# Performance work log

Hardware: AMD Instinct MI355X
Metric: run time of the kernel (lower is better)

Reference implementation:

```python
import jax, jax.numpy as jnp
import numpy as np

N, R, C = 128, 2304, 256  # batch of Stiefel params, each viewed as tall [r, c] (j==6 dispatch: 2304x256)


def setup_inputs() -> dict:
    key = jax.random.key(0)
    k1, k2, k3, k4, k5 = jax.random.split(key, 5)
    M0 = jax.random.normal(k1, (N, R, C), dtype=jnp.float32)
    # project onto the Stiefel manifold (orthonormal columns), as the real optimizer maintains
    M, _ = jnp.linalg.qr(M0)
    M_grad = jax.random.normal(k2, (N, R, C), dtype=jnp.float32)
    update = jax.random.normal(k3, (N, R, C), dtype=jnp.float32)  # stands in for LSTM optimizee output
    lr = jax.random.uniform(k4, (N, 1, 1), dtype=jnp.float32)      # stands in for LSTM-predicted lr
    s_lr = jax.random.uniform(k5, (1,), dtype=jnp.float32)
    return {"M": M, "M_grad": M_grad, "update": update, "lr": lr, "s_lr": s_lr}


def reference(M, M_grad, update, lr, s_lr):
    s = s_lr[0]

    def step(Mi, Gi_raw, Ui, lri):
        # othogonal_projection: G = Gi_raw - M @ sym(M^T @ Gi_raw)
        A = Mi.T @ Gi_raw                      # [c, c]
        A_sym = 0.5 * (A + A.T)
        G = Gi_raw - Mi @ A_sym                # [r, c]
        # update_R = -|lr| * s_lr * (update + G)
        P = -jnp.abs(lri) * s * (Ui + G)
        # retraction: QR with sign fix, then transpose (as in step())
        Q, Rm = jnp.linalg.qr(Mi + P)          # Q: [r, c], Rm: [c, c]
        sgn = jnp.sign(jnp.sign(jnp.diagonal(Rm)) + 0.5)  # (R.diag().sign()+0.5).sign()
        return (Q * sgn[None, :]).T            # [c, r] = retraction(M, P).T

    return jax.vmap(step)(M, M_grad, update, lr[:, 0, 0])
```

## Files before the change

kernel.cpp:

```cpp
#include <hip/hip_runtime.h>
#include <hip/hip_bf16.h>
#include <stdint.h>


typedef _Float16 f16;
typedef _Float16 half4 __attribute__((ext_vector_type(4)));
typedef _Float16 half8 __attribute__((ext_vector_type(8)));
typedef float float4v __attribute__((ext_vector_type(4)));

#define AS1 __attribute__((address_space(1)))
#define AS3 __attribute__((address_space(3)))

__device__ __forceinline__ void gload_lds16(const f16* g, f16* l) {
  __builtin_amdgcn_global_load_lds((const AS1 void*)g, (AS3 void*)l, 16, 0, 0);
}

__global__ __launch_bounds__(256) void prep_kernel(
    const float* __restrict__ M, const float* __restrict__ G,
    const float* __restrict__ U, const float* __restrict__ lr,
    const float* __restrict__ sl,
    f16* __restrict__ M16, f16* __restrict__ Mt,
    f16* __restrict__ Gt,  f16* __restrict__ GU)
{
  __shared__ f16 T[256 * 72];
  const int b = blockIdx.z, mode = blockIdx.y, r0 = blockIdx.x * 64;
  const int tid = threadIdx.x;
  const size_t bin = (size_t)b * 589824;
  const float* src = (mode ? G : M) + bin + (size_t)r0 * 256;
  const float* usrc = U + bin + (size_t)r0 * 256;
  const float cb = mode ? fabsf(lr[b]) * sl[0] : 0.f;

  for (int q = 0; q < 16; ++q) {
    int idx = q * 256 + tid;
    int rr = idx >> 6, c4 = (idx & 63) * 4;
    float4 v = *(const float4*)(src + (size_t)rr * 256 + c4);
    f16 h0 = (f16)v.x, h1 = (f16)v.y, h2 = (f16)v.z, h3 = (f16)v.w;
    T[(c4 + 0) * 72 + rr] = h0;
    T[(c4 + 1) * 72 + rr] = h1;
    T[(c4 + 2) * 72 + rr] = h2;
    T[(c4 + 3) * 72 + rr] = h3;
    if (mode == 0) {
      half4 hv; hv[0] = h0; hv[1] = h1; hv[2] = h2; hv[3] = h3;
      *(half4*)(M16 + bin + (size_t)(r0 + rr) * 256 + c4) = hv;
    } else {
      float4 u = *(const float4*)(usrc + (size_t)rr * 256 + c4);
      half4 gu;
      gu[0] = (f16)(cb * (v.x + u.x));
      gu[1] = (f16)(cb * (v.y + u.y));
      gu[2] = (f16)(cb * (v.z + u.z));
      gu[3] = (f16)(cb * (v.w + u.w));
      *(half4*)(GU + bin + (size_t)(r0 + rr) * 256 + c4) = gu;
    }
  }
  __syncthreads();
  f16* dst = (mode ? Gt : Mt) + bin;
  for (int q = 0; q < 8; ++q) {
    int idx = q * 256 + tid;
    int cc = idx >> 3, r8 = (idx & 7) * 8;
    half8 hv = *(const half8*)(T + cc * 72 + r8);
    *(half8*)(dst + (size_t)cc * 2304 + r0 + r8) = hv;
  }
}

__global__ __launch_bounds__(256) void tranb_kernel(const f16* __restrict__ B,
                                                    f16* __restrict__ Bt)
{
  __shared__ f16 T[256 * 72];
  const int b = blockIdx.z, r0 = blockIdx.x * 64, tid = threadIdx.x;
  const size_t bin = (size_t)b * 589824;
  for (int q = 0; q < 8; ++q) {
    int idx = q * 256 + tid;
    int rr = idx >> 5, c8 = (idx & 31) * 8;
    half8 v = *(const half8*)(B + bin + (size_t)(r0 + rr) * 256 + c8);
#pragma unroll
    for (int i = 0; i < 8; ++i) T[(c8 + i) * 72 + rr] = v[i];
  }
  __syncthreads();
  for (int q = 0; q < 8; ++q) {
    int idx = q * 256 + tid;
    int cc = idx >> 3, r8 = (idx & 7) * 8;
    *(half8*)(Bt + bin + (size_t)cc * 2304 + r0 + r8) =
        *(const half8*)(T + cc * 72 + r8);
  }
}

__global__ __launch_bounds__(256) void symw_kernel(
    const float* __restrict__ A, const float* __restrict__ lr,
    const float* __restrict__ sl, f16* __restrict__ W)
{
  __shared__ float T1[64 * 65];
  __shared__ float T2[64 * 65];
  const int b = blockIdx.z, tid = threadIdx.x;
  int pr = blockIdx.x;
  int ti = 0;
  while ((ti + 1) * (ti + 2) / 2 <= pr) ++ti;
  int tj = pr - ti * (ti + 1) / 2;
  const int i0 = ti * 64, j0 = tj * 64;
  const float* Ab = A + (size_t)b * 65536;
  const float ch = 0.5f * fabsf(lr[b]) * sl[0];

  for (int q = 0; q < 4; ++q) {
    int idx = q * 256 + tid;
    int r = idx >> 4, c4 = (idx & 15) * 4;
    float4 v = *(const float4*)(Ab + (size_t)(i0 + r) * 256 + j0 + c4);
    T1[r * 65 + c4 + 0] = v.x; T1[r * 65 + c4 + 1] = v.y;
    T1[r * 65 + c4 + 2] = v.z; T1[r * 65 + c4 + 3] = v.w;
    if (ti != tj) {
      float4 w = *(const float4*)(Ab + (size_t)(j0 + r) * 256 + i0 + c4);
      T2[r * 65 + c4 + 0] = w.x; T2[r * 65 + c4 + 1] = w.y;
      T2[r * 65 + c4 + 2] = w.z; T2[r * 65 + c4 + 3] = w.w;
    }
  }
  __syncthreads();
  const float* T2p = (ti == tj) ? T1 : T2;
  f16* Wb = W + (size_t)b * 65536;
  for (int q = 0; q < 16; ++q) {
    int idx = q * 256 + tid;
    int r = idx >> 6, c = idx & 63;
    float val = ch * (T1[r * 65 + c] + T2p[c * 65 + r]);
    if (ti == tj && r == c) val += 1.f;
    Wb[(size_t)(i0 + r) * 256 + j0 + c] = (f16)val;
  }
  if (ti != tj) {
    for (int q = 0; q < 16; ++q) {
      int idx = q * 256 + tid;
      int r = idx >> 6, c = idx & 63;
      float val = ch * (T2[r * 65 + c] + T1[c * 65 + r]);
      Wb[(size_t)(j0 + r) * 256 + i0 + c] = (f16)val;
    }
  }
}

template <int EPI>
__global__ __launch_bounds__(256) void gemm_kernel(
    const f16* __restrict__ Abase, long sA, int lda,
    const f16* __restrict__ Bbase, long sB, int ldb, int K,
    float* __restrict__ Cf, long sC, int ldc,
    f16* __restrict__ C16, const f16* __restrict__ GU, long sGU)
{
  __shared__ f16 As[128 * 64];
  __shared__ f16 Bs[128 * 64];
  const int b = blockIdx.z;
  const int tid = threadIdx.x, lane = tid & 63, wave = tid >> 6;
  const int wm = wave >> 1, wn = wave & 1;
  const int quad = lane >> 4, l15 = lane & 15;
  const f16* Ap = Abase + (size_t)b * sA + (size_t)(blockIdx.x * 128) * lda;
  const f16* Bp = Bbase + (size_t)b * sB + (size_t)(blockIdx.y * 128) * ldb;

  float4v acc[4][4];
#pragma unroll
  for (int i = 0; i < 4; ++i)
#pragma unroll
    for (int j = 0; j < 4; ++j)
#pragma unroll
      for (int r = 0; r < 4; ++r) acc[i][j][r] = 0.f;

  for (int kt = 0; kt < K; kt += 64) {
    __syncthreads();
#pragma unroll
    for (int q = 0; q < 4; ++q) {
      int pos = q * 256 + wave * 64 + lane;
      int m = pos >> 3, jc = pos & 7;
      int g = jc ^ (m & 7);
      gload_lds16(Ap + (size_t)m * lda + kt + g * 8,
                  As + (q * 256 + wave * 64) * 8);
      gload_lds16(Bp + (size_t)m * ldb + kt + g * 8,
                  Bs + (q * 256 + wave * 64) * 8);
    }
    __syncthreads();
#pragma unroll
    for (int ks = 0; ks < 2; ++ks) {
      half8 af[4], bf[4];
      int kc = ks * 4 + quad;
#pragma unroll
      for (int i = 0; i < 4; ++i) {
        int m = wm * 64 + i * 16 + l15;
        af[i] = *(const half8*)(As + m * 64 + ((kc ^ (m & 7)) * 8));
        int n = wn * 64 + i * 16 + l15;
        bf[i] = *(const half8*)(Bs + n * 64 + ((kc ^ (n & 7)) * 8));
      }
#pragma unroll
      for (int i = 0; i < 4; ++i)
#pragma unroll
        for (int j = 0; j < 4; ++j)
          acc[i][j] = __builtin_amdgcn_mfma_f32_16x16x32_f16(af[i], bf[j],
                                                             acc[i][j], 0, 0, 0);
    }
  }

#pragma unroll
  for (int i = 0; i < 4; ++i) {
#pragma unroll
    for (int j = 0; j < 4; ++j) {
      int m0 = blockIdx.x * 128 + wm * 64 + i * 16 + quad * 4;
      int n = blockIdx.y * 128 + wn * 64 + j * 16 + l15;
#pragma unroll
      for (int r = 0; r < 4; ++r) {
        int m = m0 + r;
        if constexpr (EPI == 0) {
          Cf[(size_t)b * sC + (size_t)m * ldc + n] = acc[i][j][r];
        } else {
          float v = acc[i][j][r] - (float)GU[(size_t)b * sGU + (size_t)m * 256 + n];
          C16[(size_t)b * sC + (size_t)m * ldc + n] = (f16)v;
        }
      }
    }
  }
}

__global__ __launch_bounds__(1024) void chol_kernel(float* __restrict__ Sg,
                                                    f16* __restrict__ Linv)
{
  __shared__ float Pan[256 * 32];
  __shared__ float Dinv[8 * 528];
  __shared__ float Tscr[32 * 32];
  __shared__ float stash[32];
  const int b = blockIdx.x, tid = threadIdx.x;
  float* Lg = Sg + (size_t)b * 65536;
  f16* Lo = Linv + (size_t)b * 65536;

  for (int t = tid; t < 16384; t += 1024) ((uint64_t*)Lo)[t] = 0ull;

  for (int p = 0; p < 8; ++p) {
    const int c0 = p * 32, rows = 256 - c0;
    __syncthreads();
    for (int t = tid; t < rows * 32; t += 1024) {
      int r = t >> 5, k = t & 31;
      Pan[t] = Lg[(size_t)(c0 + r) * 256 + c0 + k];
    }
    __syncthreads();
    for (int jj = 0; jj < 32; ++jj) {
      int i = jj + tid;
      bool act = (i < rows);
      int i2 = act ? i : jj;
      float pv = Pan[jj * 32 + jj];
      float v = Pan[i2 * 32 + jj];
      for (int k = 0; k < jj; ++k) {
        float ljk = Pan[jj * 32 + k];
        pv -= ljk * ljk;
        v -= Pan[i2 * 32 + k] * ljk;
      }
      float d = sqrtf(fmaxf(pv, 1e-20f));
      float rd = 1.f / d;
      if (act) {
        if (tid == 0) stash[jj] = d;
        else Pan[i * 32 + jj] = v * rd;
      }
      __syncthreads();
    }
    if (tid < 32) Pan[tid * 32 + tid] = stash[tid];
    __syncthreads();
    for (int t = tid; t < rows * 32; t += 1024) {
      int r = t >> 5, k = t & 31;
      Lg[(size_t)(c0 + r) * 256 + c0 + k] = Pan[t];
    }
    int R = 256 - (c0 + 32);
    if (R > 0) {
      int nb = R >> 3, nblk = nb * (nb + 1) / 2;
      for (int bx = tid; bx < nblk; bx += 1024) {
        int br = (int)((sqrtf(8.f * bx + 1.f) - 1.f) * 0.5f);
        while ((br + 1) * (br + 2) / 2 <= bx) ++br;
        while (br * (br + 1) / 2 > bx) --br;
        int bc = bx - br * (br + 1) / 2;
        int il = 32 + br * 8, jl = 32 + bc * 8;
        float acc[8][8];
#pragma unroll
        for (int r = 0; r < 8; ++r) {
          const float* cp = Lg + (size_t)(c0 + il + r) * 256 + c0 + jl;
#pragma unroll
          for (int c = 0; c < 8; ++c) acc[r][c] = cp[c];
        }
        for (int k = 0; k < 32; ++k) {
          float a[8], bb[8];
#pragma unroll
          for (int r = 0; r < 8; ++r) a[r] = Pan[(il + r) * 32 + k];
#pragma unroll
          for (int c = 0; c < 8; ++c) bb[c] = Pan[(jl + c) * 32 + k];
#pragma unroll
          for (int r = 0; r < 8; ++r)
#pragma unroll
            for (int c = 0; c < 8; ++c) acc[r][c] -= a[r] * bb[c];
        }
#pragma unroll
        for (int r = 0; r < 8; ++r) {
          float* cp = Lg + (size_t)(c0 + il + r) * 256 + c0 + jl;
#pragma unroll
          for (int c = 0; c < 8; ++c) cp[c] = acc[r][c];
        }
      }
    }
  }
  __syncthreads();

  if (tid < 256) {
    int w = tid >> 5, c = tid & 31;
    const float* Lb = Lg + (size_t)(32 * w) * 256 + 32 * w;
    for (int i = c; i < 32; ++i) {
      float s = (i == c) ? 1.f : 0.f;
      for (int k = c; k < i; ++k)
        s -= Lb[i * 256 + k] * Dinv[w * 528 + k * (k + 1) / 2 + c];
      Dinv[w * 528 + i * (i + 1) / 2 + c] = s / Lb[i * 256 + i];
    }
  }
  __syncthreads();

  for (int p = 0; p < 8; ++p) {
    {
      int i = tid >> 5, k = tid & 31;
      float val = (k <= i) ? Dinv[p * 528 + i * (i + 1) / 2 + k] : 0.f;
      Pan[i * 32 + k] = val;
      Lo[(size_t)(32 * p + i) * 256 + 32 * p + k] = (f16)val;
    }
    __syncthreads();
    for (int r = p + 1; r < 8; ++r) {
      int i = tid >> 5, j = tid & 31;
      float s = 0.f;
      for (int a = p; a < r; ++a) {
        const float* Lrow = Lg + (size_t)(32 * r + i) * 256 + 32 * a;
        const float* Xp = Pan + ((a - p) * 32) * 32 + j;
        for (int kk = 0; kk < 32; ++kk) s += Lrow[kk] * Xp[kk * 32];
      }
      Tscr[i * 32 + j] = s;
      __syncthreads();
      float val = 0.f;
      for (int kk = 0; kk <= i; ++kk)
        val -= Dinv[r * 528 + i * (i + 1) / 2 + kk] * Tscr[kk * 32 + j];
      Pan[((r - p) * 32 + i) * 32 + j] = val;
      Lo[(size_t)(32 * r + i) * 256 + 32 * p + j] = (f16)val;
      __syncthreads();
    }
  }
}

extern "C" void kernel_launch(void* const* d_in, const int* in_sizes, int n_in,
                              void* d_out, int out_size, void* d_ws,
                              size_t ws_size, hipStream_t stream) {
  const float* M = (const float*)d_in[0];
  const float* G = (const float*)d_in[1];
  const float* U = (const float*)d_in[2];
  const float* lr = (const float*)d_in[3];
  const float* sl = (const float*)d_in[4];
  float* out = (float*)d_out;

  const size_t big = (size_t)128 * 2304 * 256;
  char* ws = (char*)d_ws;
  size_t off = 0;
  auto alloc = [&](size_t bytes) -> char* {
    char* p = ws + off;
    off += (bytes + 255) & ~(size_t)255;
    return p;
  };
  f16* M16 = (f16*)alloc(big * 2);
  f16* Mt  = (f16*)alloc(big * 2);
  f16* Gt  = (f16*)alloc(big * 2);
  f16* GU  = (f16*)alloc(big * 2);
  f16* W   = (f16*)alloc((size_t)128 * 65536 * 2);
  float* AR = (float*)alloc((size_t)128 * 65536 * 4);

  f16* B16 = Mt;
  f16* Bt = Gt;
  float* S = AR;
  f16* LINV = W;

  dim3 blk(256);
  prep_kernel<<<dim3(36, 2, 128), blk, 0, stream>>>(M, G, U, lr, sl, M16, Mt,
                                                    Gt, GU);
  gemm_kernel<0><<<dim3(2, 2, 128), blk, 0, stream>>>(
      Mt, 589824, 2304, Gt, 589824, 2304, 2304, AR, 65536, 256, nullptr,
      nullptr, 0);
  symw_kernel<<<dim3(10, 1, 128), blk, 0, stream>>>(AR, lr, sl, W);
  gemm_kernel<1><<<dim3(18, 2, 128), blk, 0, stream>>>(
      M16, 589824, 256, W, 65536, 256, 256, nullptr, 589824, 256, B16, GU,
      589824);
  tranb_kernel<<<dim3(36, 1, 128), blk, 0, stream>>>(B16, Bt);
  gemm_kernel<0><<<dim3(2, 2, 128), blk, 0, stream>>>(
      Bt, 589824, 2304, Bt, 589824, 2304, 2304, S, 65536, 256, nullptr,
      nullptr, 0);
  chol_kernel<<<dim3(128), dim3(1024), 0, stream>>>(S, LINV);
  gemm_kernel<0><<<dim3(2, 18, 128), blk, 0, stream>>>(
      LINV, 65536, 256, B16, 589824, 256, 256, out, 589824, 2304, nullptr,
      nullptr, 0);
}
```

Measured before the change: 2.070 ms.

## Factor Cholesky panel diagonal in registers with shuffles, then row-parallel triangular solve

Replaces the per-column panel factorization, which used 32 block-wide barriers per panel, with two phases. A single wavefront factors the 32x32 diagonal block in registers using cross-lane shuffles. Each remaining row then does its own triangular solve against that block, with one barrier per phase. It also pads the panel in shared memory to stride 33 to avoid bank conflicts. In exchange, the row solves use 32-float register arrays and have serial dependency chains per thread.

```diff
diff --git a/kernel.cpp b/kernel.cpp
--- a/kernel.cpp
+++ b/kernel.cpp
@@ -211,10 +211,10 @@
 __global__ __launch_bounds__(1024) void chol_kernel(float* __restrict__ Sg,
                                                     f16* __restrict__ Linv)
 {
-  __shared__ float Pan[256 * 32];
+  __shared__ float Pan[256 * 33];
   __shared__ float Dinv[8 * 528];
   __shared__ float Tscr[32 * 32];
-  __shared__ float stash[32];
+  __shared__ float rdg[32];
   const int b = blockIdx.x, tid = threadIdx.x;
   float* Lg = Sg + (size_t)b * 65536;
   f16* Lo = Linv + (size_t)b * 65536;
@@ -226,33 +226,59 @@
     __syncthreads();
     for (int t = tid; t < rows * 32; t += 1024) {
       int r = t >> 5, k = t & 31;
-      Pan[t] = Lg[(size_t)(c0 + r) * 256 + c0 + k];
-    }
-    __syncthreads();
-    for (int jj = 0; jj < 32; ++jj) {
-      int i = jj + tid;
-      bool act = (i < rows);
-      int i2 = act ? i : jj;
-      float pv = Pan[jj * 32 + jj];
-      float v = Pan[i2 * 32 + jj];
-      for (int k = 0; k < jj; ++k) {
-        float ljk = Pan[jj * 32 + k];
-        pv -= ljk * ljk;
-        v -= Pan[i2 * 32 + k] * ljk;
-      }
-      float d = sqrtf(fmaxf(pv, 1e-20f));
-      float rd = 1.f / d;
-      if (act) {
-        if (tid == 0) stash[jj] = d;
-        else Pan[i * 32 + jj] = v * rd;
-      }
-      __syncthreads();
-    }
-    if (tid < 32) Pan[tid * 32 + tid] = stash[tid];
-    __syncthreads();
+      Pan[r * 33 + k] = Lg[(size_t)(c0 + r) * 256 + c0 + k];
+    }
+    __syncthreads();
+
+    if (tid < 64) {
+      const int i = tid & 31;
+      float a[32];
+#pragma unroll
+      for (int k = 0; k < 32; ++k) a[k] = Pan[i * 33 + k];
+#pragma unroll
+      for (int jj = 0; jj < 32; ++jj) {
+        float pv = __shfl(a[jj], jj);
+        float d = sqrtf(fmaxf(pv, 1e-20f));
+        float rd = 1.f / d;
+        float lij = (i == jj) ? d : a[jj] * rd;
+        a[jj] = lij;
+        if (tid == jj) rdg[jj] = rd;
+#pragma unroll
+        for (int k = jj + 1; k < 32; ++k) {
+          float ckj = __shfl(lij, k);
+          a[k] -= lij * ckj;
+        }
+      }
+      if (tid < 32) {
+#pragma unroll
+        for (int k = 0; k < 32; ++k)
+          if (k <= i) Pan[i * 33 + k] = a[k];
+      }
+    }
+    __syncthreads();
+
+    const int nbr = rows - 32;
+    if (tid < nbr) {
+      const int r = 32 + tid;
+      float v[32];
+#pragma unroll
+      for (int k = 0; k < 32; ++k) v[k] = Pan[r * 33 + k];
+#pragma unroll
+      for (int jj = 0; jj < 32; ++jj) {
+        float x = v[jj] * rdg[jj];
+        v[jj] = x;
+#pragma unroll
+        for (int k = jj + 1; k < 32; ++k)
+          v[k] -= x * Pan[k * 33 + jj];
+      }
+#pragma unroll
+      for (int k = 0; k < 32; ++k) Pan[r * 33 + k] = v[k];
+    }
+    __syncthreads();
+
     for (int t = tid; t < rows * 32; t += 1024) {
       int r = t >> 5, k = t & 31;
-      Lg[(size_t)(c0 + r) * 256 + c0 + k] = Pan[t];
+      Lg[(size_t)(c0 + r) * 256 + c0 + k] = Pan[r * 33 + k];
     }
     int R = 256 - (c0 + 32);
     if (R > 0) {
@@ -271,15 +297,15 @@
           for (int c = 0; c < 8; ++c) acc[r][c] = cp[c];
         }
         for (int k = 0; k < 32; ++k) {
-          float a[8], bb[8];
-#pragma unroll
-          for (int r = 0; r < 8; ++r) a[r] = Pan[(il + r) * 32 + k];
-#pragma unroll
-          for (int c = 0; c < 8; ++c) bb[c] = Pan[(jl + c) * 32 + k];
+          float a2[8], bb[8];
+#pragma unroll
+          for (int r = 0; r < 8; ++r) a2[r] = Pan[(il + r) * 33 + k];
+#pragma unroll
+          for (int c = 0; c < 8; ++c) bb[c] = Pan[(jl + c) * 33 + k];
 #pragma unroll
           for (int r = 0; r < 8; ++r)
 #pragma unroll
-            for (int c = 0; c < 8; ++c) acc[r][c] -= a[r] * bb[c];
+            for (int c = 0; c < 8; ++c) acc[r][c] -= a2[r] * bb[c];
         }
 #pragma unroll
         for (int r = 0; r < 8; ++r) {
```

After: 1.981 ms. 1.05x faster.
